# Kernel tuning notes

Measured on AMD Instinct MI355X. Metric: run time of the kernel, lower is better.

Reference implementation:

```python
import jax, jax.numpy as jnp
import numpy as np

LAMBDA_COORD = 5.0
LAMBDA_NOOBJ = 0.5


def _iou(box1, box2):
    # boxes: [..., 4] in (cx, cy, w, h) format. Matches YoloLoss.IOU:
    # returns 0 when x_right < x_left or y_bottom < y_top (strict),
    # else intersection / (area1 + area2 - intersection).
    x1, y1, w1, h1 = box1[..., 0], box1[..., 1], box1[..., 2], box1[..., 3]
    x2, y2, w2, h2 = box2[..., 0], box2[..., 1], box2[..., 2], box2[..., 3]
    x_left = jnp.maximum(x1 - w1 / 2, x2 - w2 / 2)
    y_top = jnp.maximum(y1 - h1 / 2, y2 - h2 / 2)
    x_right = jnp.minimum(x1 + w1 / 2, x2 + w2 / 2)
    y_bottom = jnp.minimum(y1 + h1 / 2, y2 + h2 / 2)
    valid = jnp.logical_and(x_right >= x_left, y_bottom >= y_top)
    inter = (x_right - x_left) * (y_bottom - y_top)
    union = w1 * h1 + w2 * h2 - inter
    safe_union = jnp.where(union == 0, 1.0, union)
    return jnp.where(valid, inter / safe_union, 0.0)


def setup_inputs() -> dict:
    key = jax.random.key(0)
    k1, k2 = jax.random.split(key)
    B, S, D = 16384, 7, 30  # D = 2*5 + 20
    y = jax.random.normal(k1, (B, S, S, D), dtype=jnp.float32)
    gt = jax.random.normal(k2, (B, S, S, D), dtype=jnp.float32)
    return {"y": y, "gt": gt}


def reference(y, gt):
    pred, target = y, gt
    batch_size = pred.shape[0]
    obj = (target[..., 4] > 0).astype(pred.dtype)      # [B,S,S]
    noobj = (target[..., 4] == 0).astype(pred.dtype)   # [B,S,S]

    # class loss (mask over class channels, indices 10:)
    class_loss = jnp.sum(obj[..., None] * (target[..., 10:] - pred[..., 10:]) ** 2)

    # no-object confidence loss (channel 4, mask before responsibility edits)
    conf_loss_no_obj = jnp.sum(noobj * (target[..., 4] - pred[..., 4]) ** 2)

    # per-cell IOU of target box vs both predicted boxes
    tbox = target[..., 0:4]
    iou1 = _iou(tbox, pred[..., 0:4])   # [B,S,S]
    iou2 = _iou(tbox, pred[..., 5:9])   # [B,S,S]

    # responsibility: keep box1 iff iou1 > iou2 (ties -> box2), as in the torch loop
    resp1 = (iou1 > iou2).astype(pred.dtype)
    m1 = obj * resp1          # box1 responsible mask
    m2 = obj * (1.0 - resp1)  # box2 responsible mask

    # object confidence loss: confidence target is the IOU of the responsible box
    conf_loss_obj = jnp.sum(m1 * (iou1 - pred[..., 4]) ** 2
                            + m2 * (iou2 - pred[..., 9]) ** 2)

    # xy loss (channels 0,1 / 5,6)
    xy_loss = jnp.sum(m1 * ((target[..., 0] - pred[..., 0]) ** 2
                            + (target[..., 1] - pred[..., 1]) ** 2)
                      + m2 * ((target[..., 0] - pred[..., 5]) ** 2
                              + (target[..., 1] - pred[..., 6]) ** 2))

    # wh loss (channels 2,3 / 7,8)
    wh_loss = jnp.sum(m1 * ((target[..., 2] - pred[..., 2]) ** 2
                            + (target[..., 3] - pred[..., 3]) ** 2)
                      + m2 * ((target[..., 2] - pred[..., 7]) ** 2
                              + (target[..., 3] - pred[..., 8]) ** 2))

    total = (LAMBDA_COORD * xy_loss + LAMBDA_COORD * wh_loss
             + conf_loss_obj + LAMBDA_NOOBJ * conf_loss_no_obj
             + class_loss) / batch_size
    return total
```

## Files before the change

### kernel.cpp

```cpp
#include <hip/hip_runtime.h>

#define LAMBDA_COORD 5.0f
#define LAMBDA_NOOBJ 0.5f
#define DD 30
#define CELLS 256
#define BLOCK 256
#define F4_PER_INPUT (CELLS * DD / 4)
#define FULL_ITERS (F4_PER_INPUT / BLOCK)

__device__ __forceinline__ float iou_t(float tx, float ty, float tw, float th,
                                       float px, float py, float pw, float ph) {
    float xl = fmaxf(tx - tw * 0.5f, px - pw * 0.5f);
    float yt = fmaxf(ty - th * 0.5f, py - ph * 0.5f);
    float xr = fminf(tx + tw * 0.5f, px + pw * 0.5f);
    float yb = fminf(ty + th * 0.5f, py + ph * 0.5f);
    bool valid = (xr >= xl) && (yb >= yt);
    float inter = (xr - xl) * (yb - yt);
    float uni = tw * th + pw * ph - inter;
    float safe = (uni == 0.0f) ? 1.0f : uni;
    return valid ? (inter / safe) : 0.0f;
}

__global__ __launch_bounds__(BLOCK) void yolo_loss_kernel(
    const float* __restrict__ pred, const float* __restrict__ targ,
    float* __restrict__ out) {
    __shared__ __align__(16) float sp[CELLS * DD];
    __shared__ __align__(16) float st[CELLS * DD];
    __shared__ float wpart[BLOCK / 64];

    const int tid = threadIdx.x;
    const size_t base = (size_t)blockIdx.x * (CELLS * DD);

    const float4* gp = (const float4*)(pred + base);
    const float4* gt = (const float4*)(targ + base);
    float4* lp = (float4*)sp;
    float4* lt = (float4*)st;
#pragma unroll
    for (int i = 0; i < FULL_ITERS; ++i) {
        lp[tid + i * BLOCK] = gp[tid + i * BLOCK];
        lt[tid + i * BLOCK] = gt[tid + i * BLOCK];
    }
    {
        int i = tid + FULL_ITERS * BLOCK;
        if (i < F4_PER_INPUT) { lp[i] = gp[i]; lt[i] = gt[i]; }
    }
    __syncthreads();

    const float* p = &sp[tid * DD];
    const float* t = &st[tid * DD];

    float t4 = t[4];
    float obj = (t4 > 0.0f) ? 1.0f : 0.0f;
    float noobj = (t4 == 0.0f) ? 1.0f : 0.0f;

    float cls = 0.0f;
#pragma unroll
    for (int k = 10; k < 30; ++k) {
        float d = t[k] - p[k];
        cls += d * d;
    }
    cls *= obj;

    float d4 = t4 - p[4];
    float conf_noobj = noobj * d4 * d4;

    float tx = t[0], ty = t[1], tw = t[2], th = t[3];
    float iou1 = iou_t(tx, ty, tw, th, p[0], p[1], p[2], p[3]);
    float iou2 = iou_t(tx, ty, tw, th, p[5], p[6], p[7], p[8]);
    float resp1 = (iou1 > iou2) ? 1.0f : 0.0f;
    float m1 = obj * resp1;
    float m2 = obj * (1.0f - resp1);

    float e1 = iou1 - p[4];
    float e2 = iou2 - p[9];
    float conf_obj = m1 * e1 * e1 + m2 * e2 * e2;

    float dx1 = tx - p[0], dy1 = ty - p[1];
    float dx2 = tx - p[5], dy2 = ty - p[6];
    float xy = m1 * (dx1 * dx1 + dy1 * dy1) + m2 * (dx2 * dx2 + dy2 * dy2);

    float dw1 = tw - p[2], dh1 = th - p[3];
    float dw2 = tw - p[7], dh2 = th - p[8];
    float wh = m1 * (dw1 * dw1 + dh1 * dh1) + m2 * (dw2 * dw2 + dh2 * dh2);

    float loss = LAMBDA_COORD * (xy + wh) + conf_obj + LAMBDA_NOOBJ * conf_noobj + cls;

#pragma unroll
    for (int off = 32; off > 0; off >>= 1) loss += __shfl_down(loss, off);
    if ((tid & 63) == 0) wpart[tid >> 6] = loss;
    __syncthreads();
    if (tid == 0) {
        float s = wpart[0] + wpart[1] + wpart[2] + wpart[3];
        atomicAdd(out, s * (1.0f / 16384.0f));
    }
}

extern "C" void kernel_launch(void* const* d_in, const int* in_sizes, int n_in,
                              void* d_out, int out_size, void* d_ws, size_t ws_size,
                              hipStream_t stream) {
    const float* pred = (const float*)d_in[0];
    const float* targ = (const float*)d_in[1];
    float* out = (float*)d_out;

    hipMemsetAsync(out, 0, sizeof(float), stream);

    const int cells = in_sizes[0] / DD;
    const int grid = cells / CELLS;
    yolo_loss_kernel<<<grid, BLOCK, 0, stream>>>(pred, targ, out);
}
```

Before: 206.8 us.

## Use direct global-to-LDS loads with single-wave blocks looping over chunks

Each block is now one 64-thread wave. It walks four 64-cell chunks and stages them with global_load_lds 16-byte direct-to-LDS loads instead of loading into registers and storing to shared memory. The cross-wave shared-memory reduction goes away and there is one atomic per wave. The loads and compute within each block run in sequence with no double buffering, so latency hiding depends on occupancy across the many small blocks.

```diff
diff --git a/kernel.cpp b/kernel.cpp
--- a/kernel.cpp
+++ b/kernel.cpp
@@ -3,10 +3,17 @@
 #define LAMBDA_COORD 5.0f
 #define LAMBDA_NOOBJ 0.5f
 #define DD 30
-#define CELLS 256
-#define BLOCK 256
-#define F4_PER_INPUT (CELLS * DD / 4)
-#define FULL_ITERS (F4_PER_INPUT / BLOCK)
+#define BLOCK 64
+#define CELLS 64
+#define ITERS 4
+#define F4_PER_CHUNK (CELLS * DD / 4)
+
+typedef const __attribute__((address_space(1))) void* gas_ptr;
+typedef __attribute__((address_space(3))) void* las_ptr;
+
+__device__ __forceinline__ void glds16(const float4* g, void* l) {
+    __builtin_amdgcn_global_load_lds((gas_ptr)g, (las_ptr)l, 16, 0, 0);
+}
 
 __device__ __forceinline__ float iou_t(float tx, float ty, float tw, float th,
                                        float px, float py, float pw, float ph) {
@@ -26,73 +33,71 @@
     float* __restrict__ out) {
     __shared__ __align__(16) float sp[CELLS * DD];
     __shared__ __align__(16) float st[CELLS * DD];
-    __shared__ float wpart[BLOCK / 64];
 
     const int tid = threadIdx.x;
-    const size_t base = (size_t)blockIdx.x * (CELLS * DD);
+    float acc = 0.0f;
 
-    const float4* gp = (const float4*)(pred + base);
-    const float4* gt = (const float4*)(targ + base);
-    float4* lp = (float4*)sp;
-    float4* lt = (float4*)st;
-#pragma unroll
-    for (int i = 0; i < FULL_ITERS; ++i) {
-        lp[tid + i * BLOCK] = gp[tid + i * BLOCK];
-        lt[tid + i * BLOCK] = gt[tid + i * BLOCK];
-    }
-    {
-        int i = tid + FULL_ITERS * BLOCK;
-        if (i < F4_PER_INPUT) { lp[i] = gp[i]; lt[i] = gt[i]; }
-    }
-    __syncthreads();
+    for (int it = 0; it < ITERS; ++it) {
+        const size_t chunk = (size_t)blockIdx.x * ITERS + it;
+        const float4* gp = (const float4*)pred + chunk * F4_PER_CHUNK;
+        const float4* gt = (const float4*)targ + chunk * F4_PER_CHUNK;
 
-    const float* p = &sp[tid * DD];
-    const float* t = &st[tid * DD];
-
-    float t4 = t[4];
-    float obj = (t4 > 0.0f) ? 1.0f : 0.0f;
-    float noobj = (t4 == 0.0f) ? 1.0f : 0.0f;
-
-    float cls = 0.0f;
-#pragma unroll
-    for (int k = 10; k < 30; ++k) {
-        float d = t[k] - p[k];
-        cls += d * d;
-    }
-    cls *= obj;
-
-    float d4 = t4 - p[4];
-    float conf_noobj = noobj * d4 * d4;
-
-    float tx = t[0], ty = t[1], tw = t[2], th = t[3];
-    float iou1 = iou_t(tx, ty, tw, th, p[0], p[1], p[2], p[3]);
-    float iou2 = iou_t(tx, ty, tw, th, p[5], p[6], p[7], p[8]);
-    float resp1 = (iou1 > iou2) ? 1.0f : 0.0f;
-    float m1 = obj * resp1;
-    float m2 = obj * (1.0f - resp1);
-
-    float e1 = iou1 - p[4];
-    float e2 = iou2 - p[9];
-    float conf_obj = m1 * e1 * e1 + m2 * e2 * e2;
-
-    float dx1 = tx - p[0], dy1 = ty - p[1];
-    float dx2 = tx - p[5], dy2 = ty - p[6];
-    float xy = m1 * (dx1 * dx1 + dy1 * dy1) + m2 * (dx2 * dx2 + dy2 * dy2);
-
-    float dw1 = tw - p[2], dh1 = th - p[3];
-    float dw2 = tw - p[7], dh2 = th - p[8];
-    float wh = m1 * (dw1 * dw1 + dh1 * dh1) + m2 * (dw2 * dw2 + dh2 * dh2);
-
-    float loss = LAMBDA_COORD * (xy + wh) + conf_obj + LAMBDA_NOOBJ * conf_noobj + cls;
+        __syncthreads();
 
 #pragma unroll
-    for (int off = 32; off > 0; off >>= 1) loss += __shfl_down(loss, off);
-    if ((tid & 63) == 0) wpart[tid >> 6] = loss;
-    __syncthreads();
-    if (tid == 0) {
-        float s = wpart[0] + wpart[1] + wpart[2] + wpart[3];
-        atomicAdd(out, s * (1.0f / 16384.0f));
+        for (int j = 0; j < 7; ++j) {
+            glds16(gp + j * 64 + tid, (char*)sp + j * 1024);
+            glds16(gt + j * 64 + tid, (char*)st + j * 1024);
+        }
+        if (tid < 32) {
+            glds16(gp + 448 + tid, (char*)sp + 7 * 1024);
+            glds16(gt + 448 + tid, (char*)st + 7 * 1024);
+        }
+        __syncthreads();
+
+        const float* p = &sp[tid * DD];
+        const float* t = &st[tid * DD];
+
+        float t4 = t[4];
+        float obj = (t4 > 0.0f) ? 1.0f : 0.0f;
+        float noobj = (t4 == 0.0f) ? 1.0f : 0.0f;
+
+        float cls = 0.0f;
+#pragma unroll
+        for (int k = 10; k < 30; ++k) {
+            float d = t[k] - p[k];
+            cls += d * d;
+        }
+        cls *= obj;
+
+        float d4 = t4 - p[4];
+        float conf_noobj = noobj * d4 * d4;
+
+        float tx = t[0], ty = t[1], tw = t[2], th = t[3];
+        float iou1 = iou_t(tx, ty, tw, th, p[0], p[1], p[2], p[3]);
+        float iou2 = iou_t(tx, ty, tw, th, p[5], p[6], p[7], p[8]);
+        float resp1 = (iou1 > iou2) ? 1.0f : 0.0f;
+        float m1 = obj * resp1;
+        float m2 = obj * (1.0f - resp1);
+
+        float e1 = iou1 - p[4];
+        float e2 = iou2 - p[9];
+        float conf_obj = m1 * e1 * e1 + m2 * e2 * e2;
+
+        float dx1 = tx - p[0], dy1 = ty - p[1];
+        float dx2 = tx - p[5], dy2 = ty - p[6];
+        float xy = m1 * (dx1 * dx1 + dy1 * dy1) + m2 * (dx2 * dx2 + dy2 * dy2);
+
+        float dw1 = tw - p[2], dh1 = th - p[3];
+        float dw2 = tw - p[7], dh2 = th - p[8];
+        float wh = m1 * (dw1 * dw1 + dh1 * dh1) + m2 * (dw2 * dw2 + dh2 * dh2);
+
+        acc += LAMBDA_COORD * (xy + wh) + conf_obj + LAMBDA_NOOBJ * conf_noobj + cls;
     }
+
+#pragma unroll
+    for (int off = 32; off > 0; off >>= 1) acc += __shfl_down(acc, off);
+    if (tid == 0) atomicAdd(out, acc * (1.0f / 16384.0f));
 }
 
 extern "C" void kernel_launch(void* const* d_in, const int* in_sizes, int n_in,
@@ -105,6 +110,6 @@
     hipMemsetAsync(out, 0, sizeof(float), stream);
 
     const int cells = in_sizes[0] / DD;
-    const int grid = cells / CELLS;
+    const int grid = cells / (CELLS * ITERS);
     yolo_loss_kernel<<<grid, BLOCK, 0, stream>>>(pred, targ, out);
 }
```

Result: slower. 216.4 us (+4.7%).

## Use persistent grid with register-prefetched double-buffered small tiles

Applied to the files above, without the earlier changes.

Replaces one large block per 256 cells with a fixed grid of 2048 persistent blocks. Each block loops over 32-cell tiles and prefetches the next tile into registers while the current one is computed out of double-buffered shared memory. Shared memory per block shrinks, so more blocks can fit per CU, and global loads overlap with compute. The cost is that only 8 lanes per wave do compute each iteration, and tile counts and grid size are hardcoded to this input shape.

```diff
diff --git a/kernel.cpp b/kernel.cpp
--- a/kernel.cpp
+++ b/kernel.cpp
@@ -3,10 +3,12 @@
 #define LAMBDA_COORD 5.0f
 #define LAMBDA_NOOBJ 0.5f
 #define DD 30
-#define CELLS 256
 #define BLOCK 256
-#define F4_PER_INPUT (CELLS * DD / 4)
-#define FULL_ITERS (F4_PER_INPUT / BLOCK)
+#define TCELLS 32
+#define F4T (TCELLS * DD / 4)
+#define GRID 2048
+#define NTILES (802816 / TCELLS)
+#define NITER 13
 
 __device__ __forceinline__ float iou_t(float tx, float ty, float tw, float th,
                                        float px, float py, float pw, float ph) {
@@ -21,73 +23,91 @@
     return valid ? (inter / safe) : 0.0f;
 }
 
-__global__ __launch_bounds__(BLOCK) void yolo_loss_kernel(
+__global__ __launch_bounds__(BLOCK, 8) void yolo_loss_kernel(
     const float* __restrict__ pred, const float* __restrict__ targ,
     float* __restrict__ out) {
-    __shared__ __align__(16) float sp[CELLS * DD];
-    __shared__ __align__(16) float st[CELLS * DD];
+    __shared__ __align__(16) float sp[2][TCELLS * DD];
+    __shared__ __align__(16) float st[2][TCELLS * DD];
     __shared__ float wpart[BLOCK / 64];
 
     const int tid = threadIdx.x;
-    const size_t base = (size_t)blockIdx.x * (CELLS * DD);
+    const int bid = blockIdx.x;
+    const int li = (tid < F4T) ? tid : (F4T - 1);
 
-    const float4* gp = (const float4*)(pred + base);
-    const float4* gt = (const float4*)(targ + base);
-    float4* lp = (float4*)sp;
-    float4* lt = (float4*)st;
+    const int wv = tid >> 6, lane = tid & 63;
+    const bool is_comp = lane < (TCELLS / 4);
+    const int mycell = lane * 4 + wv;
+
+    const float4* p4 = (const float4*)pred;
+    const float4* t4p = (const float4*)targ;
+
+    float4 RP = p4[(size_t)bid * F4T + li];
+    float4 RT = t4p[(size_t)bid * F4T + li];
+
+    float acc = 0.0f;
+
+    for (int it = 0; it < NITER; ++it) {
+        const int tile = it * GRID + bid;
+        const bool active = tile < NTILES;
+        const int cur = it & 1;
+
+        if (active) {
+            ((float4*)sp[cur])[li] = RP;
+            ((float4*)st[cur])[li] = RT;
+        }
+        __syncthreads();
+
+        const int ntile = (it + 1) * GRID + bid;
+        if (it + 1 < NITER && ntile < NTILES) {
+            RP = p4[(size_t)ntile * F4T + li];
+            RT = t4p[(size_t)ntile * F4T + li];
+        }
+
+        if (active && is_comp) {
+            const float* p = &sp[cur][mycell * DD];
+            const float* t = &st[cur][mycell * DD];
+
+            float tv4 = t[4];
+            float obj = (tv4 > 0.0f) ? 1.0f : 0.0f;
+            float noobj = (tv4 == 0.0f) ? 1.0f : 0.0f;
+
+            float cls = 0.0f;
 #pragma unroll
-    for (int i = 0; i < FULL_ITERS; ++i) {
-        lp[tid + i * BLOCK] = gp[tid + i * BLOCK];
-        lt[tid + i * BLOCK] = gt[tid + i * BLOCK];
+            for (int k = 10; k < 30; ++k) {
+                float d = t[k] - p[k];
+                cls += d * d;
+            }
+            cls *= obj;
+
+            float d4 = tv4 - p[4];
+            float conf_noobj = noobj * d4 * d4;
+
+            float tx = t[0], ty = t[1], tw = t[2], th = t[3];
+            float iou1 = iou_t(tx, ty, tw, th, p[0], p[1], p[2], p[3]);
+            float iou2 = iou_t(tx, ty, tw, th, p[5], p[6], p[7], p[8]);
+            float resp1 = (iou1 > iou2) ? 1.0f : 0.0f;
+            float m1 = obj * resp1;
+            float m2 = obj * (1.0f - resp1);
+
+            float e1 = iou1 - p[4];
+            float e2 = iou2 - p[9];
+            float conf_obj = m1 * e1 * e1 + m2 * e2 * e2;
+
+            float dx1 = tx - p[0], dy1 = ty - p[1];
+            float dx2 = tx - p[5], dy2 = ty - p[6];
+            float xy = m1 * (dx1 * dx1 + dy1 * dy1) + m2 * (dx2 * dx2 + dy2 * dy2);
+
+            float dw1 = tw - p[2], dh1 = th - p[3];
+            float dw2 = tw - p[7], dh2 = th - p[8];
+            float wh = m1 * (dw1 * dw1 + dh1 * dh1) + m2 * (dw2 * dw2 + dh2 * dh2);
+
+            acc += LAMBDA_COORD * (xy + wh) + conf_obj + LAMBDA_NOOBJ * conf_noobj + cls;
+        }
     }
-    {
-        int i = tid + FULL_ITERS * BLOCK;
-        if (i < F4_PER_INPUT) { lp[i] = gp[i]; lt[i] = gt[i]; }
-    }
-    __syncthreads();
-
-    const float* p = &sp[tid * DD];
-    const float* t = &st[tid * DD];
-
-    float t4 = t[4];
-    float obj = (t4 > 0.0f) ? 1.0f : 0.0f;
-    float noobj = (t4 == 0.0f) ? 1.0f : 0.0f;
-
-    float cls = 0.0f;
-#pragma unroll
-    for (int k = 10; k < 30; ++k) {
-        float d = t[k] - p[k];
-        cls += d * d;
-    }
-    cls *= obj;
-
-    float d4 = t4 - p[4];
-    float conf_noobj = noobj * d4 * d4;
-
-    float tx = t[0], ty = t[1], tw = t[2], th = t[3];
-    float iou1 = iou_t(tx, ty, tw, th, p[0], p[1], p[2], p[3]);
-    float iou2 = iou_t(tx, ty, tw, th, p[5], p[6], p[7], p[8]);
-    float resp1 = (iou1 > iou2) ? 1.0f : 0.0f;
-    float m1 = obj * resp1;
-    float m2 = obj * (1.0f - resp1);
-
-    float e1 = iou1 - p[4];
-    float e2 = iou2 - p[9];
-    float conf_obj = m1 * e1 * e1 + m2 * e2 * e2;
-
-    float dx1 = tx - p[0], dy1 = ty - p[1];
-    float dx2 = tx - p[5], dy2 = ty - p[6];
-    float xy = m1 * (dx1 * dx1 + dy1 * dy1) + m2 * (dx2 * dx2 + dy2 * dy2);
-
-    float dw1 = tw - p[2], dh1 = th - p[3];
-    float dw2 = tw - p[7], dh2 = th - p[8];
-    float wh = m1 * (dw1 * dw1 + dh1 * dh1) + m2 * (dw2 * dw2 + dh2 * dh2);
-
-    float loss = LAMBDA_COORD * (xy + wh) + conf_obj + LAMBDA_NOOBJ * conf_noobj + cls;
 
 #pragma unroll
-    for (int off = 32; off > 0; off >>= 1) loss += __shfl_down(loss, off);
-    if ((tid & 63) == 0) wpart[tid >> 6] = loss;
+    for (int off = 32; off > 0; off >>= 1) acc += __shfl_down(acc, off);
+    if (lane == 0) wpart[wv] = acc;
     __syncthreads();
     if (tid == 0) {
         float s = wpart[0] + wpart[1] + wpart[2] + wpart[3];
@@ -104,7 +124,5 @@
 
     hipMemsetAsync(out, 0, sizeof(float), stream);
 
-    const int cells = in_sizes[0] / DD;
-    const int grid = cells / CELLS;
-    yolo_loss_kernel<<<grid, BLOCK, 0, stream>>>(pred, targ, out);
+    yolo_loss_kernel<<<GRID, BLOCK, 0, stream>>>(pred, targ, out);
 }
```

New measurement: 275.3 us. +33.1%, slower.
